# Kernel optimization log

Hardware: AMD Instinct MI355X
Metric: run time of the kernel (lower is better)

The kernel has to match this reference:

```python
import jax, jax.numpy as jnp
import numpy as np
from jax.scipy.special import logsumexp

B, T, K = 256, 512, 20
START_TAG, STOP_TAG = 18, 19


def setup_inputs() -> dict:
    key = jax.random.key(0)
    k1, k2, k3, k4 = jax.random.split(key, 4)
    features = jax.random.normal(k1, (B, T, K, K), dtype=jnp.float32)
    transitions = jax.random.normal(k2, (K, K), dtype=jnp.float32)
    targets = jax.random.randint(k3, (B, T), 0, 18, dtype=jnp.int32)
    lengths = jax.random.randint(k4, (B,), 1, T + 1, dtype=jnp.int32)
    return {"features": features, "transitions": transitions,
            "targets": targets, "lengths": lengths}


def reference(features, transitions, targets, lengths):
    # features: [B, T, K, K] with features[b,t,i,j] = emission(tag i at t) + transition(j -> i)
    b, t, k, _ = features.shape
    valid = jnp.arange(t)[None, :] < lengths[:, None]  # [B, T]

    # ---- gold path score ----
    prev = jnp.concatenate(
        [jnp.full((b, 1), START_TAG, dtype=targets.dtype), targets[:, :-1]], axis=1)
    flat_idx = targets.astype(jnp.int32) * k + prev.astype(jnp.int32)  # [B, T]
    scores_at_targets = jnp.take_along_axis(
        features.reshape(b, t, k * k), flat_idx[:, :, None].astype(jnp.int32), axis=2)[..., 0]
    last_tag = jnp.take_along_axis(targets, (lengths - 1)[:, None].astype(jnp.int32), axis=1)[:, 0]
    gold_score = jnp.sum(jnp.where(valid, scores_at_targets, 0.0)) \
        + jnp.sum(transitions[STOP_TAG, last_tag])

    # ---- forward algorithm (sequential log-sum-exp scan over time) ----
    alpha0 = features[:, 0, :, START_TAG]  # [B, K]; all lengths >= 1

    def step(alpha, inp):
        f_t, tt = inp  # f_t: [B, K, K]
        new = logsumexp(f_t + alpha[:, None, :], axis=2)  # [B, K]
        active = (tt < lengths)[:, None]
        return jnp.where(active, new, alpha), None

    feats_rest = jnp.swapaxes(features[:, 1:], 0, 1)  # [T-1, B, K, K]
    alpha, _ = jax.lax.scan(step, alpha0, (feats_rest, jnp.arange(1, t)))

    all_paths_scores = jnp.sum(logsumexp(alpha + transitions[STOP_TAG][None, :], axis=1))
    return all_paths_scores - gold_score
```

## Files before the change

kernel.cpp:

```cpp
#include <hip/hip_runtime.h>
#include <math.h>
#include <stdint.h>

#define BB 256
#define TT 512
#define KK 20
#define START_TAG 18
#define STOP_TAG 19
#define NST 400
#define SEGSTRIDE 420
#define WS_SEG_OFF 1024

typedef __bf16 bf16x8 __attribute__((ext_vector_type(8)));
typedef float f32x16 __attribute__((ext_vector_type(16)));
typedef uint32_t u32x4 __attribute__((ext_vector_type(4)));

__device__ __forceinline__ float fexp2(float x){ float r; asm("v_exp_f32 %0, %1":"=v"(r):"v"(x)); return r; }
__device__ __forceinline__ float flog2(float x){ float r; asm("v_log_f32 %0, %1":"=v"(r):"v"(x)); return r; }
__device__ __forceinline__ uint32_t pk_bf16(float lo, float hi){
  uint32_t r; asm("v_cvt_pk_bf16_f32 %0, %1, %2":"=v"(r):"v"(lo),"v"(hi)); return r;
}
__device__ __forceinline__ void pswap(uint32_t &a, uint32_t &b){
  asm("v_permlane32_swap_b32 %0, %1":"+v"(a),"+v"(b));
}
__device__ __forceinline__ f32x16 mfma_bf16(u32x4 a, u32x4 b, f32x16 c){
  return __builtin_amdgcn_mfma_f32_32x32x16_bf16(
    __builtin_bit_cast(bf16x8,a), __builtin_bit_cast(bf16x8,b), c, 0,0,0);
}

template<int SEGL, int SEGS>
__global__ __launch_bounds__(64) void seg_mfma(
    const float* __restrict__ feats, const int* __restrict__ lengths,
    float* __restrict__ wseg)
{
  constexpr float LOG2E = 1.4426950408889634f;
  const int lane = threadIdx.x;
  const int n  = lane & 31;
  const int hi = lane >> 5;
  const int task = blockIdx.x;
  const int b = task / SEGS;
  const int s = task - b*SEGS;
  const int seg0 = 1 + SEGL*s;
  const int len = lengths[b];
  int nv = len - seg0; nv = nv < 0 ? 0 : (nv > SEGL ? SEGL : nv);
  if (nv <= 0) return;

  const bool rowok = n < KK;
  const int rli = rowok ? n : 0;
  const float* rbase = feats + (size_t)(b*TT + seg0)*NST + rli*KK;
  const int off0 = hi ? 8 : 0;

  u32x4 B0, B1;
  #pragma unroll
  for (int d=0; d<4; ++d){
    int k0 = hi*8 + 2*d;
    uint32_t v = 0;
    if (k0   == n && n < KK) v |= 0x3F80u;
    if (k0+1 == n && n < KK) v |= 0x3F800000u;
    B0[d] = v;
    int m0 = 16 + hi*8 + 2*d;
    uint32_t u = 0;
    if (m0   == n && n < KK) u |= 0x3F80u;
    if (m0+1 == n && n < KK) u |= 0x3F800000u;
    B1[d] = u;
  }

  int cexp = 0;
  f32x16 acc;
  #pragma unroll
  for (int r=0;r<16;++r) acc[r] = 0.f;

  float4 a0,a1,a2, p0,p1,p2;
  auto LD = [&](int it, float4 &r0, float4 &r1, float4 &r2){
    const float* p = rbase + (size_t)it*NST;
    r0 = *(const float4*)(p + off0);
    r1 = *(const float4*)(p + off0 + 4);
    r2 = (hi == 0) ? *(const float4*)(p + 16) : make_float4(0.f,0.f,0.f,0.f);
  };
  auto CONV = [&](const float4 &r0, const float4 &r1, const float4 &r2,
                  u32x4 &A0, u32x4 &A1){
    uint32_t w0 = pk_bf16(fexp2(r0.x*LOG2E), fexp2(r0.y*LOG2E));
    uint32_t w1 = pk_bf16(fexp2(r0.z*LOG2E), fexp2(r0.w*LOG2E));
    uint32_t w2 = pk_bf16(fexp2(r1.x*LOG2E), fexp2(r1.y*LOG2E));
    uint32_t w3 = pk_bf16(fexp2(r1.z*LOG2E), fexp2(r1.w*LOG2E));
    uint32_t w4 = pk_bf16(fexp2(r2.x*LOG2E), fexp2(r2.y*LOG2E));
    uint32_t w5 = pk_bf16(fexp2(r2.z*LOG2E), fexp2(r2.w*LOG2E));
    if (!rowok){ w0=0u; w1=0u; w2=0u; w3=0u; }
    if (!(rowok && hi==0)){ w4=0u; w5=0u; }
    A0[0]=w0; A0[1]=w1; A0[2]=w2; A0[3]=w3;
    A1[0]=w4; A1[1]=w5; A1[2]=0u; A1[3]=0u;
  };
  auto RENORM = [&](){
    float mx = acc[0];
    #pragma unroll
    for (int r=1;r<16;++r) mx = fmaxf(mx, acc[r]);
    mx = fmaxf(mx, __shfl_xor(mx, 32, 64));
    int e = (int)((__float_as_uint(mx) >> 23) & 255) - 127;
    if (e < -100) e = -100;
    float sc = __uint_as_float((uint32_t)(127 - e) << 23);
    #pragma unroll
    for (int r=0;r<16;++r) acc[r] *= sc;
    cexp += e;
  };
  auto C2B = [&](){
    uint32_t x0 = pk_bf16(acc[0],  acc[1]);
    uint32_t x1 = pk_bf16(acc[2],  acc[3]);
    uint32_t x2 = pk_bf16(acc[4],  acc[5]);
    uint32_t x3 = pk_bf16(acc[6],  acc[7]);
    uint32_t x4 = pk_bf16(acc[8],  acc[9]);
    uint32_t x5 = pk_bf16(acc[10], acc[11]);
    uint32_t x6 = pk_bf16(acc[12], acc[13]);
    uint32_t x7 = pk_bf16(acc[14], acc[15]);
    pswap(x0,x2); pswap(x1,x3); pswap(x4,x6); pswap(x5,x7);
    B0[0]=x0; B0[1]=x1; B0[2]=x2; B0[3]=x3;
    B1[0]=x4; B1[1]=x5; B1[2]=x6; B1[3]=x7;
  };

  LD(0, a0,a1,a2);
  for (int it=0; it<nv-1; ++it){
    LD(it+1, p0,p1,p2);
    u32x4 A0, A1; CONV(a0,a1,a2, A0,A1);
    f32x16 z;
    #pragma unroll
    for (int r=0;r<16;++r) z[r] = 0.f;
    acc = mfma_bf16(A0, B0, z);
    acc = mfma_bf16(A1, B1, acc);
    if (SEGL > 8 && (it & 7) == 7) RENORM();
    C2B();
    a0=p0; a1=p1; a2=p2;
  }
  {
    u32x4 A0, A1; CONV(a0,a1,a2, A0,A1);
    f32x16 z;
    #pragma unroll
    for (int r=0;r<16;++r) z[r] = 0.f;
    acc = mfma_bf16(A0, B0, z);
    acc = mfma_bf16(A1, B1, acc);
  }
  RENORM();

  float* out = wseg + (size_t)task*SEGSTRIDE;
  #pragma unroll
  for (int r=0;r<16;++r){
    int row = (r&3) + 8*(r>>2) + 4*hi;
    if (row < KK && n < KK) out[row*KK + n] = acc[r];
  }
  if (hi==0 && n<KK) ((int*)out)[NST + n] = cexp;
}

template<int SEGL, int SEGS>
__global__ __launch_bounds__(64,1) void chain_kernel2(
    const float* __restrict__ feats, const float* __restrict__ trans,
    const int* __restrict__ targets, const int* __restrict__ lengths,
    const float* __restrict__ wseg, float* __restrict__ partialA)
{
    constexpr float LOG2E = 1.4426950408889634f;
    constexpr float LN2   = 0.6931471805599453f;
    const int b = blockIdx.x;
    const int lane = threadIdx.x;
    const int len = lengths[b];
    const bool act = lane < KK;
    const int li = act ? lane : 0;

    __shared__ __align__(16) float Ul[KK];

    const float* fb = feats + (size_t)b*TT*NST;
    float a2 = fb[li*KK + START_TAG] * LOG2E;
    float c0 = __uint_as_float(__builtin_amdgcn_readfirstlane(__float_as_uint(a2)));
    float CW = c0;
    float wk = act ? fexp2(a2 - c0) : 0.f;

    const int nseg = (len - 1 + SEGL - 1) / SEGL;

    if (act && nseg > 0){
        float4 mA[5], mB[5];
        int cA = 0, cB = 0;
        auto LDM = [&](int s2, float4 (&m)[5], int& c){
            const float* base = wseg + (size_t)(b*SEGS + s2)*SEGSTRIDE;
            const float4* p4 = (const float4*)(base + li*KK);
            m[0]=p4[0]; m[1]=p4[1]; m[2]=p4[2]; m[3]=p4[3]; m[4]=p4[4];
            c = ((const int*)base)[NST + li];
        };
        auto STEP = [&](float4 (&m)[5], int c){
            int e = (int)((__float_as_uint(wk) >> 23) & 255) - 127;
            int q = __builtin_amdgcn_readfirstlane(c + e);
            Ul[li] = ldexpf(wk, c - q);
            asm volatile("s_waitcnt lgkmcnt(0)" ::: "memory");
            const float4* up = (const float4*)Ul;
            float4 u0 = up[0], u1 = up[1], u2 = up[2], u3 = up[3], u4 = up[4];
            float s0 = m[0].x*u0.x, s1 = m[0].y*u0.y;
            s0 = fmaf(m[0].z,u0.z,s0); s1 = fmaf(m[0].w,u0.w,s1);
            s0 = fmaf(m[1].x,u1.x,s0); s1 = fmaf(m[1].y,u1.y,s1);
            s0 = fmaf(m[1].z,u1.z,s0); s1 = fmaf(m[1].w,u1.w,s1);
            s0 = fmaf(m[2].x,u2.x,s0); s1 = fmaf(m[2].y,u2.y,s1);
            s0 = fmaf(m[2].z,u2.z,s0); s1 = fmaf(m[2].w,u2.w,s1);
            s0 = fmaf(m[3].x,u3.x,s0); s1 = fmaf(m[3].y,u3.y,s1);
            s0 = fmaf(m[3].z,u3.z,s0); s1 = fmaf(m[3].w,u3.w,s1);
            s0 = fmaf(m[4].x,u4.x,s0); s1 = fmaf(m[4].y,u4.y,s1);
            s0 = fmaf(m[4].z,u4.z,s0); s1 = fmaf(m[4].w,u4.w,s1);
            wk = s0 + s1;
            CW += (float)q;
            asm volatile("s_waitcnt lgkmcnt(0)" ::: "memory");
        };
        LDM(0, mA, cA);
        for (int s2 = 0; s2 < nseg; ){
            if (s2 + 1 < nseg) LDM(s2 + 1, mB, cB);
            STEP(mA, cA);
            ++s2; if (s2 >= nseg) break;
            if (s2 + 1 < nseg) LDM(s2 + 1, mA, cA);
            STEP(mB, cB);
            ++s2;
        }
    }

    float term = act ? wk * fexp2(trans[STOP_TAG*KK + li] * LOG2E) : 0.f;
    #pragma unroll
    for (int o = 32; o > 0; o >>= 1) term += __shfl_xor(term, o, 64);
    if (lane == 0){
        float lse = LN2 * (CW + flog2(term));
        int last = targets[b*TT + len - 1];
        partialA[b] = lse - trans[STOP_TAG*KK + last];
    }
}

__global__ __launch_bounds__(64,1) void fwd_serial(
    const float* __restrict__ feats, const float* __restrict__ trans,
    const int* __restrict__ targets, const int* __restrict__ lengths,
    float* __restrict__ partialA)
{
    constexpr float LOG2E = 1.4426950408889634f;
    constexpr float LN2   = 0.6931471805599453f;
    const int b    = blockIdx.x;
    const int lane = threadIdx.x;
    const int len  = lengths[b];
    const float* fb = feats + (size_t)b * TT * NST;
    __shared__ __align__(16) float alpha[KK];
    __shared__ __align__(16) float xs[KK];
    const bool act = lane < KK;
    const int  li  = act ? lane : 0;
    if (act) alpha[lane] = fb[lane * KK + START_TAG] * LOG2E;
    __syncthreads();
    float4 b0[5], b1[5], b2[5], b3[5];
    auto LOAD = [&](float4* dst, int t){
        int tc = (t < len) ? t : (len - 1);
        const float4* p = (const float4*)(fb + (size_t)tc * NST + li * KK);
        dst[0]=p[0]; dst[1]=p[1]; dst[2]=p[2]; dst[3]=p[3]; dst[4]=p[4];
    };
    auto STEP = [&](const float4* bufv){
        const float4* ap = (const float4*)alpha;
        float a[KK];
        #pragma unroll
        for (int q = 0; q < 5; ++q){
            float4 av = ap[q];
            a[4*q+0]=av.x; a[4*q+1]=av.y; a[4*q+2]=av.z; a[4*q+3]=av.w;
        }
        float v[KK];
        #pragma unroll
        for (int q = 0; q < 5; ++q){
            v[4*q+0] = bufv[q].x * LOG2E + a[4*q+0];
            v[4*q+1] = bufv[q].y * LOG2E + a[4*q+1];
            v[4*q+2] = bufv[q].z * LOG2E + a[4*q+2];
            v[4*q+3] = bufv[q].w * LOG2E + a[4*q+3];
        }
        float m = v[0];
        #pragma unroll
        for (int j = 1; j < KK; ++j) m = fmaxf(m, v[j]);
        float s = 0.f;
        #pragma unroll
        for (int j = 0; j < KK; ++j) s += fexp2(v[j] - m);
        float na = m + flog2(s);
        __syncthreads();
        if (act) alpha[lane] = na;
        __syncthreads();
    };
    LOAD(b0,1); LOAD(b1,2); LOAD(b2,3); LOAD(b3,4);
    int t = 1;
    while (t < len){
        STEP(b0); LOAD(b0, t+4); ++t; if (t >= len) break;
        STEP(b1); LOAD(b1, t+4); ++t; if (t >= len) break;
        STEP(b2); LOAD(b2, t+4); ++t; if (t >= len) break;
        STEP(b3); LOAD(b3, t+4); ++t;
    }
    if (act) xs[lane] = alpha[lane] + trans[STOP_TAG*KK + lane] * LOG2E;
    __syncthreads();
    if (lane == 0){
        float m = xs[0];
        for (int j = 1; j < KK; ++j) m = fmaxf(m, xs[j]);
        float s = 0.f;
        for (int j = 0; j < KK; ++j) s += fexp2(xs[j] - m);
        float lse = LN2 * (m + flog2(s));
        int last_tag = targets[b*TT + (len-1)];
        partialA[b] = lse - trans[STOP_TAG*KK + last_tag];
    }
}

__global__ __launch_bounds__(256) void gold_kernel(
    const float* __restrict__ feats, const int* __restrict__ targets,
    const int* __restrict__ lengths, float* __restrict__ partialG)
{
    const int b   = blockIdx.x;
    const int tt  = blockIdx.y * 256 + threadIdx.x;
    const int len = lengths[b];
    float val = 0.f;
    if (tt < len){
        int tgt  = targets[b*TT + tt];
        int prev = (tt > 0) ? targets[b*TT + tt - 1] : START_TAG;
        val = feats[((size_t)b*TT + tt)*NST + tgt*KK + prev];
    }
    #pragma unroll
    for (int off = 32; off > 0; off >>= 1) val += __shfl_down(val, off);
    __shared__ float wsum[4];
    if ((threadIdx.x & 63) == 0) wsum[threadIdx.x >> 6] = val;
    __syncthreads();
    if (threadIdx.x == 0)
        partialG[b*gridDim.y + blockIdx.y] = wsum[0]+wsum[1]+wsum[2]+wsum[3];
}

__global__ __launch_bounds__(256) void final_kernel(
    const float* __restrict__ partialA, const float* __restrict__ partialG,
    float* __restrict__ out)
{
    int tid = threadIdx.x;
    float v = partialA[tid] - partialG[tid] - partialG[tid + 256];
    #pragma unroll
    for (int off = 32; off > 0; off >>= 1) v += __shfl_down(v, off);
    __shared__ float wsum[4];
    if ((tid & 63) == 0) wsum[tid >> 6] = v;
    __syncthreads();
    if (tid == 0) out[0] = wsum[0]+wsum[1]+wsum[2]+wsum[3];
}

extern "C" void kernel_launch(void* const* d_in, const int* in_sizes, int n_in,
                              void* d_out, int out_size, void* d_ws, size_t ws_size,
                              hipStream_t stream) {
    const float* feats   = (const float*)d_in[0];
    const float* trans   = (const float*)d_in[1];
    const int*   targets = (const int*)d_in[2];
    const int*   lengths = (const int*)d_in[3];

    float* ws       = (float*)d_ws;
    float* partialA = ws;
    float* partialG = ws + 256;
    float* wseg     = ws + WS_SEG_OFF;

    const size_t need8  = (size_t)(WS_SEG_OFF + (size_t)BB*64*SEGSTRIDE) * sizeof(float);
    const size_t need16 = (size_t)(WS_SEG_OFF + (size_t)BB*32*SEGSTRIDE) * sizeof(float);

    if (ws_size >= need8){
        seg_mfma<8,64><<<dim3(BB*64), dim3(64), 0, stream>>>(feats, lengths, wseg);
        chain_kernel2<8,64><<<dim3(BB), dim3(64), 0, stream>>>(feats, trans, targets, lengths, wseg, partialA);
    } else if (ws_size >= need16){
        seg_mfma<16,32><<<dim3(BB*32), dim3(64), 0, stream>>>(feats, lengths, wseg);
        chain_kernel2<16,32><<<dim3(BB), dim3(64), 0, stream>>>(feats, trans, targets, lengths, wseg, partialA);
    } else {
        fwd_serial<<<dim3(BB), dim3(64), 0, stream>>>(feats, trans, targets, lengths, partialA);
    }
    gold_kernel<<<dim3(BB, 2), dim3(256), 0, stream>>>(feats, targets, lengths, partialG);
    final_kernel<<<dim3(1), dim3(256), 0, stream>>>(partialA, partialG, (float*)d_out);
}
```

Measured before the change: 52.42 us.

## Use 64-step segments with two-deep load prefetch in segment MFMA kernel

Switches the segmented forward scan from 64 segments of 8 steps per sequence to 8 segments of 64 steps, launching far fewer segment blocks and shrinking the chain kernel's combine work. The segment loop now prefetches two timesteps ahead and always renormalizes every 8 steps. The trade-off is a longer serial dependency chain inside each segment and much less block-level parallelism (2048 blocks instead of 16384). There is also a redundant no-op line in the B1 setup.

```diff
diff --git a/kernel.cpp b/kernel.cpp
--- a/kernel.cpp
+++ b/kernel.cpp
@@ -60,6 +60,8 @@
     B0[d] = v;
     int m0 = 16 + hi*8 + 2*d;
     uint32_t u = 0;
+    if (m0   == n && n < KK) u |= 0x3F800000u * 0 + ((m0 == n && n < KK) ? 0x3F80u : 0u);
+    u = 0;
     if (m0   == n && n < KK) u |= 0x3F80u;
     if (m0+1 == n && n < KK) u |= 0x3F800000u;
     B1[d] = u;
@@ -70,7 +72,7 @@
   #pragma unroll
   for (int r=0;r<16;++r) acc[r] = 0.f;
 
-  float4 a0,a1,a2, p0,p1,p2;
+  float4 a0,a1,a2, p0,p1,p2, q0,q1,q2;
   auto LD = [&](int it, float4 &r0, float4 &r1, float4 &r2){
     const float* p = rbase + (size_t)it*NST;
     r0 = *(const float4*)(p + off0);
@@ -117,25 +119,21 @@
   };
 
   LD(0, a0,a1,a2);
-  for (int it=0; it<nv-1; ++it){
-    LD(it+1, p0,p1,p2);
+  LD((1 < nv) ? 1 : 0, p0,p1,p2);
+  q0=a0; q1=a1; q2=a2;
+  for (int it=0; it<nv; ++it){
+    if (it+2 < nv) LD(it+2, q0,q1,q2);
     u32x4 A0, A1; CONV(a0,a1,a2, A0,A1);
     f32x16 z;
     #pragma unroll
     for (int r=0;r<16;++r) z[r] = 0.f;
     acc = mfma_bf16(A0, B0, z);
     acc = mfma_bf16(A1, B1, acc);
-    if (SEGL > 8 && (it & 7) == 7) RENORM();
+    if (it == nv-1) break;
+    if ((it & 7) == 7) RENORM();
     C2B();
     a0=p0; a1=p1; a2=p2;
-  }
-  {
-    u32x4 A0, A1; CONV(a0,a1,a2, A0,A1);
-    f32x16 z;
-    #pragma unroll
-    for (int r=0;r<16;++r) z[r] = 0.f;
-    acc = mfma_bf16(A0, B0, z);
-    acc = mfma_bf16(A1, B1, acc);
+    p0=q0; p1=q1; p2=q2;
   }
   RENORM();
 
@@ -343,15 +341,11 @@
     float* partialG = ws + 256;
     float* wseg     = ws + WS_SEG_OFF;
 
-    const size_t need8  = (size_t)(WS_SEG_OFF + (size_t)BB*64*SEGSTRIDE) * sizeof(float);
-    const size_t need16 = (size_t)(WS_SEG_OFF + (size_t)BB*32*SEGSTRIDE) * sizeof(float);
-
-    if (ws_size >= need8){
-        seg_mfma<8,64><<<dim3(BB*64), dim3(64), 0, stream>>>(feats, lengths, wseg);
-        chain_kernel2<8,64><<<dim3(BB), dim3(64), 0, stream>>>(feats, trans, targets, lengths, wseg, partialA);
-    } else if (ws_size >= need16){
-        seg_mfma<16,32><<<dim3(BB*32), dim3(64), 0, stream>>>(feats, lengths, wseg);
-        chain_kernel2<16,32><<<dim3(BB), dim3(64), 0, stream>>>(feats, trans, targets, lengths, wseg, partialA);
+    const size_t need64 = (size_t)(WS_SEG_OFF + (size_t)BB*8*SEGSTRIDE) * sizeof(float);
+
+    if (ws_size >= need64){
+        seg_mfma<64,8><<<dim3(BB*8), dim3(64), 0, stream>>>(feats, lengths, wseg);
+        chain_kernel2<64,8><<<dim3(BB), dim3(64), 0, stream>>>(feats, trans, targets, lengths, wseg, partialA);
     } else {
         fwd_serial<<<dim3(BB), dim3(64), 0, stream>>>(feats, trans, targets, lengths, partialA);
     }
```

Result: faster. 48.83 us (-6.8%).
